# Optimization experiments

Measured on AMD Instinct MI355X. Metric: run time of the kernel, lower is better.

Reference implementation:

```python
import jax, jax.numpy as jnp
import numpy as np

N_GENES = 15135
K = int(np.ceil(0.5 * N_GENES))  # 7568, PyG TopKPooling ratio=0.5
BS, E, F_IN, H, HF, NC, L = 8, 242160, 64, 128, 512, 2, 3


def setup_inputs() -> dict:
    key = jax.random.key(0)
    ks = jax.random.split(key, 16)
    def lin(k, fin, fout):
        s = 1.0 / np.sqrt(fin)
        return jax.random.normal(k, (fin, fout), jnp.float32) * s
    x = jax.random.normal(ks[0], (BS, N_GENES, F_IN), jnp.float32)
    batch = jnp.zeros((BS,), jnp.int32)
    edge_index = jax.random.randint(ks[1], (2, E), 0, N_GENES, dtype=jnp.int32)
    CAT = L * H
    return {
        "x": x,
        "batch": batch,
        "edge_index": edge_index,
        "W1": lin(ks[2], F_IN, H), "b1": jnp.zeros((H,), jnp.float32),
        "W2": lin(ks[3], H, H),    "b2": jnp.zeros((H,), jnp.float32),
        "W3": lin(ks[4], H, H),    "b3": jnp.zeros((H,), jnp.float32),
        "topk_w": jax.random.normal(ks[5], (CAT,), jnp.float32) / np.sqrt(CAT),
        "fcW": lin(ks[6], CAT, 1), "fcb": jnp.zeros((1,), jnp.float32),
        "lin1W": lin(ks[7], K, HF), "lin1b": jnp.zeros((HF,), jnp.float32),
        "lin2W": lin(ks[8], HF, NC), "lin2b": jnp.zeros((NC,), jnp.float32),
    }


def reference(x, batch, edge_index, W1, b1, W2, b2, W3, b3,
              topk_w, fcW, fcb, lin1W, lin1b, lin2W, lin2b):
    bs = x.shape[0]
    # --- GCN normalization with self-loops (PyG GCNConv defaults) ---
    loop = jnp.arange(N_GENES, dtype=edge_index.dtype)
    src = jnp.concatenate([edge_index[0], loop])
    dst = jnp.concatenate([edge_index[1], loop])
    deg = jnp.zeros((N_GENES,), x.dtype).at[dst].add(1.0)
    dinv = jax.lax.rsqrt(deg)  # deg >= 1 due to self-loops
    norm = dinv[src] * dinv[dst]  # [E+N]

    def gcn(h, W, b):
        h = h @ W                                   # [bs, N, H]
        msg = h[:, src, :] * norm[None, :, None]    # gather + edge weight
        agg = jnp.zeros_like(h).at[:, dst, :].add(msg)  # scatter-add
        return agg + b

    h1 = jax.nn.relu(gcn(x, W1, b1))
    h2 = jax.nn.relu(gcn(h1, W2, b2))
    h3 = jax.nn.relu(gcn(h2, W3, b3))
    # mode='cat': stack on last dim then flatten -> feature order (H, layer)
    xc = jnp.stack([h1, h2, h3], -1).reshape(bs, N_GENES, -1)  # [bs, N, L*H]

    # --- TopKPooling (score = tanh(x.w/||w||), keep top ceil(0.5*N)) ---
    score = jnp.tanh((xc @ topk_w) / jnp.linalg.norm(topk_w))  # [bs, N]
    top_s, perm = jax.lax.top_k(score, K)                       # [bs, K]
    xp = jnp.take_along_axis(xc, perm[..., None], axis=1) * top_s[..., None]

    z = (xp @ fcW + fcb)[..., 0]          # [bs, K]
    h = jax.nn.relu(z @ lin1W + lin1b)    # [bs, HF]; dropout inactive (eval)
    logits = h @ lin2W + lin2b            # [bs, NC]
    return jax.nn.log_softmax(logits, axis=-1)
```

## Files before the change

### kernel.cpp

```cpp
#include <hip/hip_runtime.h>
#include <hip/hip_fp16.h>

#define N_G   15135
#define E_N   242160
#define BSZ   8
#define K_TOP 7568
#define NH    128
#define NBIN  65536
#define SUFS  65600

typedef float f4v __attribute__((ext_vector_type(4)));
typedef unsigned int u4v __attribute__((ext_vector_type(4)));

__global__ void zero_kernel(int* __restrict__ p, int n) {
  int i = blockIdx.x * 1024 + threadIdx.x;
  if (i < n) p[i] = 0;
}

__global__ void count_kernel(const int* __restrict__ ei, int* __restrict__ cnt) {
  int e = blockIdx.x * 256 + threadIdx.x;
  if (e < E_N) atomicAdd(&cnt[ei[E_N + e]], 1);
}

__global__ __launch_bounds__(1024) void scan_kernel(const int* __restrict__ cnt,
                                                    int* __restrict__ rowstart,
                                                    float* __restrict__ dinv,
                                                    int4* __restrict__ rowdesc,
                                                    int* __restrict__ gctr,
                                                    const float* __restrict__ topk_w,
                                                    float* __restrict__ scal) {
  __shared__ int buf[1024];
  __shared__ int base;
  int tid = threadIdx.x;
  int i = blockIdx.x * 1024 + tid;
  int v = (i < N_G) ? cnt[i] : 0;
  float di = 1.0f / sqrtf((float)(v + 1));
  if (i < N_G) dinv[i] = di;
  buf[tid] = v;
  __syncthreads();
  for (int s = 1; s < 1024; s <<= 1) {
    int t = (tid >= s) ? buf[tid - s] : 0;
    __syncthreads();
    buf[tid] += t;
    __syncthreads();
  }
  if (tid == 1023) base = atomicAdd(gctr, buf[1023]);
  __syncthreads();
  if (i < N_G) {
    int rs = base + buf[tid] - v;
    rowstart[i] = rs;
    rowdesc[i] = make_int4(rs, v, __float_as_int(di), 0);
  }
  if (blockIdx.x == 0) {
    __shared__ float fbuf[512];
    if (tid < 512) {
      float w = (tid < 384) ? topk_w[tid] : 0.f;
      fbuf[tid] = w * w;
    }
    __syncthreads();
    for (int s = 256; s > 0; s >>= 1) {
      if (tid < s) fbuf[tid] += fbuf[tid + s];
      __syncthreads();
    }
    if (tid == 0) scal[0] = 1.0f / sqrtf(fbuf[0]);
  }
}

__global__ void fill_kernel(const int* __restrict__ ei, const int* __restrict__ rowstart,
                            const float* __restrict__ dinv, int* __restrict__ fillc,
                            int2* __restrict__ csr) {
  int e = blockIdx.x * 256 + threadIdx.x;
  if (e < E_N) {
    int s = ei[e], d = ei[E_N + e];
    int pos = rowstart[d] + atomicAdd(&fillc[d], 1);
    csr[pos] = make_int2(s, __float_as_int(dinv[s]));
  }
}

template<int CIN, bool BR, bool H16>
__global__ __launch_bounds__(256, 6) void mm_kernel(const float* __restrict__ A,
                                                    const float* __restrict__ W,
                                                    const float* __restrict__ bias,
                                                    void* __restrict__ outv) {
  __shared__ float Bst[32][132];
  __shared__ float Ast2[32][68];
  int tid = threadIdx.x;
  int b = blockIdx.x & 7;
  int ib = blockIdx.x >> 3;
  int rb0 = b * N_G + ib * 64;
  int rmax = N_G - ib * 64;
  int c0 = (tid & 31) * 4;
  int r0 = (tid >> 5) * 8;
  float acc[8][4];
#pragma unroll
  for (int i = 0; i < 8; i++)
#pragma unroll
    for (int j = 0; j < 4; j++) acc[i][j] = 0.f;

  for (int k0 = 0; k0 < CIN; k0 += 32) {
    {
      int koff = (tid & 7) * 4;
      int row = tid >> 3;
#pragma unroll
      for (int p = 0; p < 2; ++p) {
        int r = row + p * 32;
        f4v v = {0.f, 0.f, 0.f, 0.f};
        if (r < rmax) v = __builtin_nontemporal_load((const f4v*)(A + (size_t)(rb0 + r) * CIN + k0 + koff));
        Ast2[koff + 0][r] = v.x; Ast2[koff + 1][r] = v.y;
        Ast2[koff + 2][r] = v.z; Ast2[koff + 3][r] = v.w;
      }
    }
    {
      int cc = (tid & 31) * 4;
      int kr = tid >> 5;
#pragma unroll
      for (int p = 0; p < 4; ++p) {
        int k = kr + p * 8;
        *(float4*)&Bst[k][cc] = *(const float4*)(W + (size_t)(k0 + k) * NH + cc);
      }
    }
    __syncthreads();
#pragma unroll 4
    for (int kk = 0; kk < 32; ++kk) {
      float a[8], bb[4];
      *(float4*)&a[0] = *(const float4*)&Ast2[kk][r0];
      *(float4*)&a[4] = *(const float4*)&Ast2[kk][r0 + 4];
      *(float4*)&bb[0] = *(const float4*)&Bst[kk][c0];
#pragma unroll
      for (int i = 0; i < 8; i++)
#pragma unroll
        for (int j = 0; j < 4; j++)
          acc[i][j] = fmaf(a[i], bb[j], acc[i][j]);
    }
    __syncthreads();
  }
  float b0 = 0.f, b1 = 0.f, b2 = 0.f, b3 = 0.f;
  if (BR) { b0 = bias[c0]; b1 = bias[c0+1]; b2 = bias[c0+2]; b3 = bias[c0+3]; }
#pragma unroll
  for (int i = 0; i < 8; i++) {
    int r = r0 + i;
    if (r < rmax) {
      if (H16) {
        __half2 pr[2];
        pr[0] = __floats2half2_rn(acc[i][0], acc[i][1]);
        pr[1] = __floats2half2_rn(acc[i][2], acc[i][3]);
        *(uint2*)((__half*)outv + (size_t)(rb0 + r) * NH + c0) = *(uint2*)pr;
      } else {
        float4 v;
        if (BR) {
          v.x = fmaxf(acc[i][0] + b0, 0.f); v.y = fmaxf(acc[i][1] + b1, 0.f);
          v.z = fmaxf(acc[i][2] + b2, 0.f); v.w = fmaxf(acc[i][3] + b3, 0.f);
        } else {
          v.x = acc[i][0]; v.y = acc[i][1]; v.z = acc[i][2]; v.w = acc[i][3];
        }
        *(float4*)((float*)outv + (size_t)(rb0 + r) * NH + c0) = v;
      }
    }
  }
}

__global__ __launch_bounds__(256) void agg64_f4_kernel(const float* __restrict__ src,
                                                       const int2* __restrict__ csr,
                                                       const int4* __restrict__ rowdesc,
                                                       float* __restrict__ dst) {
  int b = blockIdx.x & 7;
  int chunk = blockIdx.x >> 3;
  int wave = threadIdx.x >> 6, lane = threadIdx.x & 63;
  int d = chunk * 4 + wave;
  if (d >= N_G) return;
  d = __builtin_amdgcn_readfirstlane(d);
  int slot = lane >> 4, li = lane & 15;
  int4 rd = rowdesc[d];
  int n = rd.y;
  float dv = __int_as_float(rd.z);
  const float* sb = src + (size_t)b * N_G * 64;
  const int2* ce = csr + rd.x;
  auto sel4 = [&](int a0, int a1, int a2, int a3) {
    int s01 = (slot & 1) ? a1 : a0;
    int s23 = (slot & 1) ? a3 : a2;
    return (slot & 2) ? s23 : s01;
  };
  f4v acc0 = {0.f, 0.f, 0.f, 0.f}, acc1 = {0.f, 0.f, 0.f, 0.f};
  {
    f4v sv = *(const f4v*)(sb + (size_t)d * 64 + li * 4);
    float ws = (slot == 0) ? dv : 0.f;
    acc0.x = fmaf(ws, sv.x, acc0.x); acc0.y = fmaf(ws, sv.y, acc0.y);
    acc0.z = fmaf(ws, sv.z, acc0.z); acc0.w = fmaf(ws, sv.w, acc0.w);
  }
  int l = 0;
  for (; l + 8 <= n; l += 8) {
    int2 p[8];
#pragma unroll
    for (int k = 0; k < 8; ++k) p[k] = ce[l + k];
    int s0 = sel4(p[0].x, p[1].x, p[2].x, p[3].x);
    int s1 = sel4(p[4].x, p[5].x, p[6].x, p[7].x);
    float w0 = __int_as_float(sel4(p[0].y, p[1].y, p[2].y, p[3].y));
    float w1 = __int_as_float(sel4(p[4].y, p[5].y, p[6].y, p[7].y));
    f4v v0 = *(const f4v*)(sb + (size_t)s0 * 64 + li * 4);
    f4v v1 = *(const f4v*)(sb + (size_t)s1 * 64 + li * 4);
    acc0.x = fmaf(w0, v0.x, acc0.x); acc0.y = fmaf(w0, v0.y, acc0.y);
    acc0.z = fmaf(w0, v0.z, acc0.z); acc0.w = fmaf(w0, v0.w, acc0.w);
    acc1.x = fmaf(w1, v1.x, acc1.x); acc1.y = fmaf(w1, v1.y, acc1.y);
    acc1.z = fmaf(w1, v1.z, acc1.z); acc1.w = fmaf(w1, v1.w, acc1.w);
  }
  for (; l < n; ++l) {
    int2 p = ce[l];
    float w = (slot == 0) ? __int_as_float(p.y) : 0.f;
    f4v v = *(const f4v*)(sb + (size_t)p.x * 64 + li * 4);
    acc0.x = fmaf(w, v.x, acc0.x); acc0.y = fmaf(w, v.y, acc0.y);
    acc0.z = fmaf(w, v.z, acc0.z); acc0.w = fmaf(w, v.w, acc0.w);
  }
  f4v a;
  a.x = acc0.x + acc1.x; a.y = acc0.y + acc1.y;
  a.z = acc0.z + acc1.z; a.w = acc0.w + acc1.w;
  a.x += __shfl_xor(a.x, 16); a.y += __shfl_xor(a.y, 16);
  a.z += __shfl_xor(a.z, 16); a.w += __shfl_xor(a.w, 16);
  a.x += __shfl_xor(a.x, 32); a.y += __shfl_xor(a.y, 32);
  a.z += __shfl_xor(a.z, 32); a.w += __shfl_xor(a.w, 32);
  if (slot == 0) {
    f4v r;
    r.x = dv * a.x; r.y = dv * a.y; r.z = dv * a.z; r.w = dv * a.w;
    __builtin_nontemporal_store(r, (f4v*)(dst + ((size_t)b * N_G + d) * 64 + li * 4));
  }
}

__global__ __launch_bounds__(256) void agg128_f4_kernel(const float* __restrict__ hw,
                                                        const int2* __restrict__ csr,
                                                        const int4* __restrict__ rowdesc,
                                                        const float* __restrict__ bias,
                                                        float* __restrict__ hout) {
  int b = blockIdx.x & 7;
  int chunk = blockIdx.x >> 3;
  int wave = threadIdx.x >> 6, lane = threadIdx.x & 63;
  int d0 = chunk * 8 + wave * 2;
  if (d0 >= N_G) return;
  d0 = __builtin_amdgcn_readfirstlane(d0);
  int d1i = d0 + 1;
  int has1 = (d1i < N_G);
  int dB = has1 ? d1i : d0;
  int half = lane >> 5, li = lane & 31;
  int4 rdA = rowdesc[d0];
  int4 rdB = rowdesc[dB];
  int nA = rdA.y, nB = has1 ? rdB.y : 0;
  float dvA = __int_as_float(rdA.z);
  float dvB = __int_as_float(rdB.z);
  const float* sb = hw + (size_t)b * N_G * NH;
  const int2* ceA = csr + rdA.x;
  const int2* ceB = csr + rdB.x;
  auto sel2 = [&](int a0, int a1) { return half ? a1 : a0; };
  f4v aA0 = {0.f,0.f,0.f,0.f}, aA1 = {0.f,0.f,0.f,0.f};
  f4v aB0 = {0.f,0.f,0.f,0.f}, aB1 = {0.f,0.f,0.f,0.f};
  {
    f4v sv = *(const f4v*)(sb + (size_t)d0 * NH + li * 4);
    float ws = (half == 0) ? dvA : 0.f;
    aA0.x = fmaf(ws, sv.x, aA0.x); aA0.y = fmaf(ws, sv.y, aA0.y);
    aA0.z = fmaf(ws, sv.z, aA0.z); aA0.w = fmaf(ws, sv.w, aA0.w);
    f4v svb = *(const f4v*)(sb + (size_t)dB * NH + li * 4);
    float wsb = (half == 0 && has1) ? dvB : 0.f;
    aB0.x = fmaf(wsb, svb.x, aB0.x); aB0.y = fmaf(wsb, svb.y, aB0.y);
    aB0.z = fmaf(wsb, svb.z, aB0.z); aB0.w = fmaf(wsb, svb.w, aB0.w);
  }
  auto batch8 = [&](const int2* ce, int l, f4v& c0, f4v& c1) {
    int2 p[8];
#pragma unroll
    for (int k = 0; k < 8; ++k) p[k] = ce[l + k];
    int s0 = sel2(p[0].x, p[1].x), s1 = sel2(p[2].x, p[3].x);
    int s2 = sel2(p[4].x, p[5].x), s3 = sel2(p[6].x, p[7].x);
    float w0 = __int_as_float(sel2(p[0].y, p[1].y));
    float w1 = __int_as_float(sel2(p[2].y, p[3].y));
    float w2 = __int_as_float(sel2(p[4].y, p[5].y));
    float w3 = __int_as_float(sel2(p[6].y, p[7].y));
    f4v v0 = *(const f4v*)(sb + (size_t)s0 * NH + li * 4);
    f4v v1 = *(const f4v*)(sb + (size_t)s1 * NH + li * 4);
    f4v v2 = *(const f4v*)(sb + (size_t)s2 * NH + li * 4);
    f4v v3 = *(const f4v*)(sb + (size_t)s3 * NH + li * 4);
    c0.x = fmaf(w0, v0.x, c0.x); c0.y = fmaf(w0, v0.y, c0.y);
    c0.z = fmaf(w0, v0.z, c0.z); c0.w = fmaf(w0, v0.w, c0.w);
    c1.x = fmaf(w1, v1.x, c1.x); c1.y = fmaf(w1, v1.y, c1.y);
    c1.z = fmaf(w1, v1.z, c1.z); c1.w = fmaf(w1, v1.w, c1.w);
    c0.x = fmaf(w2, v2.x, c0.x); c0.y = fmaf(w2, v2.y, c0.y);
    c0.z = fmaf(w2, v2.z, c0.z); c0.w = fmaf(w2, v2.w, c0.w);
    c1.x = fmaf(w3, v3.x, c1.x); c1.y = fmaf(w3, v3.y, c1.y);
    c1.z = fmaf(w3, v3.z, c1.z); c1.w = fmaf(w3, v3.w, c1.w);
  };
  int lA = 0, lB = 0;
  while (lA + 8 <= nA && lB + 8 <= nB) {
    batch8(ceA, lA, aA0, aA1);
    batch8(ceB, lB, aB0, aB1);
    lA += 8; lB += 8;
  }
  for (; lA + 8 <= nA; lA += 8) batch8(ceA, lA, aA0, aA1);
  for (; lB + 8 <= nB; lB += 8) batch8(ceB, lB, aB0, aB1);
  while (lA < nA || lB < nB) {
    int hasA = (lA < nA), hasB = (lB < nB);
    int sA = hasA ? ceA[lA].x : d0;
    int wAi = hasA ? ceA[lA].y : 0;
    int sB = hasB ? ceB[lB].x : d0;
    int wBi = hasB ? ceB[lB].y : 0;
    int s = half ? sB : sA;
    float wa = (half == 0 && hasA) ? __int_as_float(wAi) : 0.f;
    float wb = (half == 1 && hasB) ? __int_as_float(wBi) : 0.f;
    f4v v = *(const f4v*)(sb + (size_t)s * NH + li * 4);
    aA0.x = fmaf(wa, v.x, aA0.x); aA0.y = fmaf(wa, v.y, aA0.y);
    aA0.z = fmaf(wa, v.z, aA0.z); aA0.w = fmaf(wa, v.w, aA0.w);
    aB0.x = fmaf(wb, v.x, aB0.x); aB0.y = fmaf(wb, v.y, aB0.y);
    aB0.z = fmaf(wb, v.z, aB0.z); aB0.w = fmaf(wb, v.w, aB0.w);
    lA += hasA; lB += hasB;
  }
  f4v aA, aB;
  aA.x = aA0.x + aA1.x; aA.y = aA0.y + aA1.y;
  aA.z = aA0.z + aA1.z; aA.w = aA0.w + aA1.w;
  aB.x = aB0.x + aB1.x; aB.y = aB0.y + aB1.y;
  aB.z = aB0.z + aB1.z; aB.w = aB0.w + aB1.w;
  aA.x += __shfl_xor(aA.x, 32); aA.y += __shfl_xor(aA.y, 32);
  aA.z += __shfl_xor(aA.z, 32); aA.w += __shfl_xor(aA.w, 32);
  aB.x += __shfl_xor(aB.x, 32); aB.y += __shfl_xor(aB.y, 32);
  aB.z += __shfl_xor(aB.z, 32); aB.w += __shfl_xor(aB.w, 32);

  f4v bb = *(const f4v*)(bias + li * 4);
  float dv = half ? dvB : dvA;
  f4v av;
  av.x = half ? aB.x : aA.x; av.y = half ? aB.y : aA.y;
  av.z = half ? aB.z : aA.z; av.w = half ? aB.w : aA.w;
  f4v r;
  r.x = fmaxf(fmaf(dv, av.x, bb.x), 0.f);
  r.y = fmaxf(fmaf(dv, av.y, bb.y), 0.f);
  r.z = fmaxf(fmaf(dv, av.z, bb.z), 0.f);
  r.w = fmaxf(fmaf(dv, av.w, bb.w), 0.f);
  int dsel = half ? dB : d0;
  if (half == 0 || has1)
    __builtin_nontemporal_store(r, (f4v*)(hout + ((size_t)b * N_G + dsel) * NH + li * 4));
}

__global__ __launch_bounds__(256) void agg128h_score_kernel(
    const __half* __restrict__ hwh,
    const int2* __restrict__ csr,
    const int4* __restrict__ rowdesc,
    const float* __restrict__ bias,
    const float* __restrict__ h1,
    const float* __restrict__ h2,
    const float* __restrict__ topk_w,
    const float* __restrict__ fcW,
    const float* __restrict__ scal,
    float* __restrict__ score,
    float* __restrict__ d2a,
    unsigned* __restrict__ keys,
    int* __restrict__ hist) {
  int b = blockIdx.x & 7;
  int chunk = blockIdx.x >> 3;
  int wave = threadIdx.x >> 6, lane = threadIdx.x & 63;
  int d = chunk * 4 + wave;
  if (d >= N_G) return;
  d = __builtin_amdgcn_readfirstlane(d);
  int slot = lane >> 4, li = lane & 15;
  int4 rd = rowdesc[d];
  int n = rd.y;
  float dv = __int_as_float(rd.z);
  const __half* sb = hwh + (size_t)b * N_G * NH;
  const int2* ce = csr + rd.x;
  auto sel4 = [&](int a0, int a1, int a2, int a3) {
    int s01 = (slot & 1) ? a1 : a0;
    int s23 = (slot & 1) ? a3 : a2;
    return (slot & 2) ? s23 : s01;
  };
  float a0[8], a1[8];
#pragma unroll
  for (int j = 0; j < 8; ++j) { a0[j] = 0.f; a1[j] = 0.f; }
  auto gacc = [&](int s, float w, float* acc) {
    u4v raw = *(const u4v*)(sb + (size_t)s * NH + li * 8);
    unsigned q0 = raw.x, q1 = raw.y, q2 = raw.z, q3 = raw.w;
    float2 f0 = __half22float2(*(const __half2*)&q0);
    float2 f1 = __half22float2(*(const __half2*)&q1);
    float2 f2 = __half22float2(*(const __half2*)&q2);
    float2 f3 = __half22float2(*(const __half2*)&q3);
    acc[0] = fmaf(w, f0.x, acc[0]); acc[1] = fmaf(w, f0.y, acc[1]);
    acc[2] = fmaf(w, f1.x, acc[2]); acc[3] = fmaf(w, f1.y, acc[3]);
    acc[4] = fmaf(w, f2.x, acc[4]); acc[5] = fmaf(w, f2.y, acc[5]);
    acc[6] = fmaf(w, f3.x, acc[6]); acc[7] = fmaf(w, f3.y, acc[7]);
  };
  gacc(d, (slot == 0) ? dv : 0.f, a0);
  int l = 0;
  for (; l + 8 <= n; l += 8) {
    int2 p[8];
#pragma unroll
    for (int k = 0; k < 8; ++k) p[k] = ce[l + k];
    int s0 = sel4(p[0].x, p[1].x, p[2].x, p[3].x);
    int s1 = sel4(p[4].x, p[5].x, p[6].x, p[7].x);
    float w0 = __int_as_float(sel4(p[0].y, p[1].y, p[2].y, p[3].y));
    float w1 = __int_as_float(sel4(p[4].y, p[5].y, p[6].y, p[7].y));
    gacc(s0, w0, a0);
    gacc(s1, w1, a1);
  }
  for (; l < n; ++l) {
    int2 p = ce[l];
    gacc(p.x, (slot == 0) ? __int_as_float(p.y) : 0.f, a0);
  }
  float a[8];
#pragma unroll
  for (int j = 0; j < 8; ++j) {
    a[j] = a0[j] + a1[j];
    a[j] += __shfl_xor(a[j], 16);
    a[j] += __shfl_xor(a[j], 32);
  }
  size_t rb = ((size_t)b * N_G + d) * NH + li * 8;
  f4v u1a = __builtin_nontemporal_load((const f4v*)(h1 + rb));
  f4v u1b = __builtin_nontemporal_load((const f4v*)(h1 + rb + 4));
  f4v u2a = __builtin_nontemporal_load((const f4v*)(h2 + rb));
  f4v u2b = __builtin_nontemporal_load((const f4v*)(h2 + rb + 4));
  f4v bba = *(const f4v*)(bias + li * 8);
  f4v bbb = *(const f4v*)(bias + li * 8 + 4);
  float r[8];
  r[0] = fmaxf(fmaf(dv, a[0], bba.x), 0.f);
  r[1] = fmaxf(fmaf(dv, a[1], bba.y), 0.f);
  r[2] = fmaxf(fmaf(dv, a[2], bba.z), 0.f);
  r[3] = fmaxf(fmaf(dv, a[3], bba.w), 0.f);
  r[4] = fmaxf(fmaf(dv, a[4], bbb.x), 0.f);
  r[5] = fmaxf(fmaf(dv, a[5], bbb.y), 0.f);
  r[6] = fmaxf(fmaf(dv, a[6], bbb.z), 0.f);
  r[7] = fmaxf(fmaf(dv, a[7], bbb.w), 0.f);
  float u1[8] = {u1a.x, u1a.y, u1a.z, u1a.w, u1b.x, u1b.y, u1b.z, u1b.w};
  float u2[8] = {u2a.x, u2a.y, u2a.z, u2a.w, u2b.x, u2b.y, u2b.z, u2b.w};
  const float* tw = topk_w + li * 24;
  const float* fw = fcW + li * 24;
  float d1 = 0.f, d2 = 0.f;
#pragma unroll
  for (int j = 0; j < 8; ++j) {
    d1 += u1[j] * tw[j * 3] + u2[j] * tw[j * 3 + 1] + r[j] * tw[j * 3 + 2];
    d2 += u1[j] * fw[j * 3] + u2[j] * fw[j * 3 + 1] + r[j] * fw[j * 3 + 2];
  }
#pragma unroll
  for (int sh = 8; sh > 0; sh >>= 1) {
    d1 += __shfl_down(d1, sh, 16);
    d2 += __shfl_down(d2, sh, 16);
  }
  if (lane == 0) {
    int gw = b * N_G + d;
    float scv = tanhf(d1 * scal[0]);
    score[gw] = scv;
    d2a[gw] = d2;
    unsigned u = __float_as_uint(scv);
    unsigned k32 = (u & 0x80000000u) ? ~u : (u | 0x80000000u);
    keys[gw] = k32;
    atomicAdd(&hist[b * NBIN + (int)(k32 >> 16)], 1);
  }
}

__global__ __launch_bounds__(1024) void suffix_kernel(const int* __restrict__ hist,
                                                      int* __restrict__ suf) {
  __shared__ int buf[1024];
  int b = blockIdx.x;
  const int* hb = hist + b * NBIN;
  int* sb = suf + b * SUFS;
  int t = threadIdx.x;
  int base = t * 64;
  int s = 0;
  for (int k = 0; k < 64; ++k) s += hb[base + k];
  buf[t] = s;
  __syncthreads();
  for (int off = 1; off < 1024; off <<= 1) {
    int v = (t + off < 1024) ? buf[t + off] : 0;
    __syncthreads();
    buf[t] += v;
    __syncthreads();
  }
  int acc = buf[t] - s;
  if (t == 0) sb[NBIN] = 0;
  for (int k = 63; k >= 0; --k) {
    acc += hb[base + k];
    sb[base + k] = acc;
  }
}

__global__ void scatter_kernel(const unsigned* __restrict__ keys, int* __restrict__ hist,
                               const int* __restrict__ suf, int2* __restrict__ bucket) {
  int b = blockIdx.y;
  int i = blockIdx.x * 256 + threadIdx.x;
  if (i >= N_G) return;
  unsigned k = keys[b * N_G + i];
  int bin = (int)(k >> 16);
  int old = atomicSub(&hist[b * NBIN + bin], 1);
  int pos = suf[b * SUFS + bin + 1] + old - 1;
  bucket[b * N_G + pos] = make_int2((int)k, i);
}

__global__ void rank_z_kernel(const unsigned* __restrict__ keys, const int* __restrict__ suf,
                              const int2* __restrict__ bucket, const float* __restrict__ score,
                              const float* __restrict__ d2a, const float* __restrict__ fcb,
                              float* __restrict__ z) {
  int b = blockIdx.y;
  int i = blockIdx.x * 256 + threadIdx.x;
  if (i >= N_G) return;
  int gw = b * N_G + i;
  unsigned k = keys[gw];
  int bin = (int)(k >> 16);
  int lo = suf[b * SUFS + bin + 1];
  int hi = suf[b * SUFS + bin];
  int r = lo;
  const int2* bk = bucket + b * N_G;
  for (int p = lo; p < hi; ++p) {
    int2 e = bk[p];
    unsigned kj = (unsigned)e.x;
    r += (kj > k || (kj == k && e.y < i)) ? 1 : 0;
  }
  if (r < K_TOP) z[b * K_TOP + r] = fmaf(score[gw], d2a[gw], fcb[0]);
}

__global__ __launch_bounds__(256) void lin1_kernel(const float* __restrict__ z,
                                                   const float* __restrict__ W,
                                                   float* __restrict__ hpre) {
  __shared__ float zb[8][237];
  int rs = blockIdx.x;
  int r0 = rs * 237;
  int rn = K_TOP - r0; if (rn > 237) rn = 237;
  for (int t = threadIdx.x; t < 8 * rn; t += 256) {
    int bb = t / rn, rr = t - bb * rn;
    zb[bb][rr] = z[bb * K_TOP + r0 + rr];
  }
  __syncthreads();
  int c = threadIdx.x;
  float a[8][2];
#pragma unroll
  for (int bb = 0; bb < 8; ++bb) { a[bb][0] = 0.f; a[bb][1] = 0.f; }
  for (int r = 0; r < rn; ++r) {
    const float* wr = W + (size_t)(r0 + r) * 512;
    float w0 = wr[c], w1 = wr[c + 256];
#pragma unroll
    for (int bb = 0; bb < 8; ++bb) {
      float zz = zb[bb][r];
      a[bb][0] = fmaf(zz, w0, a[bb][0]);
      a[bb][1] = fmaf(zz, w1, a[bb][1]);
    }
  }
#pragma unroll
  for (int bb = 0; bb < 8; ++bb) {
    atomicAdd(&hpre[bb * 512 + c], a[bb][0]);
    atomicAdd(&hpre[bb * 512 + c + 256], a[bb][1]);
  }
}

__global__ __launch_bounds__(128) void lin2_kernel(const float* __restrict__ hpre,
                                                   const float* __restrict__ l1b,
                                                   const float* __restrict__ W2,
                                                   const float* __restrict__ l2b,
                                                   float* __restrict__ out) {
  int b = blockIdx.x, tid = threadIdx.x;
  float a0 = 0.f, a1 = 0.f;
  for (int j = tid; j < 512; j += 128) {
    float t = fmaxf(hpre[b * 512 + j] + l1b[j], 0.f);
    a0 = fmaf(t, W2[j * 2 + 0], a0);
    a1 = fmaf(t, W2[j * 2 + 1], a1);
  }
#pragma unroll
  for (int s = 32; s > 0; s >>= 1) {
    a0 += __shfl_down(a0, s);
    a1 += __shfl_down(a1, s);
  }
  __shared__ float red[2][2];
  if ((tid & 63) == 0) { red[tid >> 6][0] = a0; red[tid >> 6][1] = a1; }
  __syncthreads();
  if (tid == 0) {
    float l0 = red[0][0] + red[1][0] + l2b[0];
    float l1 = red[0][1] + red[1][1] + l2b[1];
    float m = fmaxf(l0, l1);
    float lse = m + logf(expf(l0 - m) + expf(l1 - m));
    out[b * 2 + 0] = l0 - lse;
    out[b * 2 + 1] = l1 - lse;
  }
}

extern "C" void kernel_launch(void* const* d_in, const int* in_sizes, int n_in,
                              void* d_out, int out_size, void* d_ws, size_t ws_size,
                              hipStream_t stream) {
  const float* x   = (const float*)d_in[0];
  const int*   ei  = (const int*)d_in[2];
  const float* W1  = (const float*)d_in[3];
  const float* b1  = (const float*)d_in[4];
  const float* W2  = (const float*)d_in[5];
  const float* b2  = (const float*)d_in[6];
  const float* W3  = (const float*)d_in[7];
  const float* b3  = (const float*)d_in[8];
  const float* tkw = (const float*)d_in[9];
  const float* fcW = (const float*)d_in[10];
  const float* fcb = (const float*)d_in[11];
  const float* l1W = (const float*)d_in[12];
  const float* l1b = (const float*)d_in[13];
  const float* l2W = (const float*)d_in[14];
  const float* l2b = (const float*)d_in[15];
  float* out = (float*)d_out;

  char* ws = (char*)d_ws;
  size_t off = 0;
  auto alloc = [&](size_t bytes) {
    char* p = ws + off;
    off += (bytes + 255) & ~(size_t)255;
    return p;
  };
  int*   cnt   = (int*)alloc(15136 * 4);
  int*   fillc = (int*)alloc(15136 * 4);
  int*   gctr  = (int*)alloc(256);
  float* hpre  = (float*)alloc(4096 * 4);
  int*   hist  = (int*)alloc((size_t)BSZ * NBIN * 4);
  int*   rowstart = (int*)alloc(15136 * 4);
  float* dinv  = (float*)alloc(15136 * 4);
  int4*  rowdesc = (int4*)alloc(15136 * 16);
  float* scal  = (float*)alloc(64);
  float* z     = (float*)alloc((size_t)BSZ * K_TOP * 4);
  float* score = (float*)alloc(121088 * 4);
  float* d2a   = (float*)alloc(121088 * 4);
  unsigned* keys = (unsigned*)alloc(121088 * 4);
  int*   suf   = (int*)alloc((size_t)BSZ * SUFS * 4);
  int2*  bucket = (int2*)alloc(121088 * 8);
  int2*  csr   = (int2*)alloc((size_t)E_N * 8);
  float* ax = (float*)alloc((size_t)BSZ * N_G * 64 * 4);
  float* hw = (float*)alloc((size_t)BSZ * N_G * NH * 4);
  float* h1 = (float*)alloc((size_t)BSZ * N_G * NH * 4);
  float* h2 = (float*)alloc((size_t)BSZ * N_G * NH * 4);
  (void)ws_size; (void)in_sizes; (void)n_in; (void)out_size;

  int zero_n = (int)(((char*)rowstart - (char*)cnt) / 4);
  zero_kernel<<<(zero_n + 1023) / 1024, 1024, 0, stream>>>(cnt, zero_n);
  count_kernel<<<(E_N + 255) / 256, 256, 0, stream>>>(ei, cnt);
  scan_kernel<<<(N_G + 1023) / 1024, 1024, 0, stream>>>(cnt, rowstart, dinv, rowdesc, gctr, tkw, scal);
  fill_kernel<<<(E_N + 255) / 256, 256, 0, stream>>>(ei, rowstart, dinv, fillc, csr);

  dim3 mmg(8 * 237);
  int aggblocks  = 8 * ((N_G + 3) / 4);
  int aggblocks2 = 8 * ((N_G + 7) / 8);

  agg64_f4_kernel<<<aggblocks, 256, 0, stream>>>(x, csr, rowdesc, ax);
  mm_kernel<64, true, false><<<mmg, 256, 0, stream>>>(ax, W1, b1, h1);
  mm_kernel<128, false, false><<<mmg, 256, 0, stream>>>(h1, W2, nullptr, hw);
  agg128_f4_kernel<<<aggblocks2, 256, 0, stream>>>(hw, csr, rowdesc, b2, h2);
  mm_kernel<128, false, true><<<mmg, 256, 0, stream>>>(h2, W3, nullptr, hw);
  agg128h_score_kernel<<<aggblocks, 256, 0, stream>>>((const __half*)hw, csr, rowdesc, b3,
                                                      h1, h2, tkw, fcW, scal,
                                                      score, d2a, keys, hist);

  dim3 ng((N_G + 255) / 256, BSZ);
  suffix_kernel<<<BSZ, 1024, 0, stream>>>(hist, suf);
  scatter_kernel<<<ng, 256, 0, stream>>>(keys, hist, suf, bucket);
  rank_z_kernel<<<ng, 256, 0, stream>>>(keys, suf, bucket, score, d2a, fcb, z);

  lin1_kernel<<<32, 256, 0, stream>>>(z, l1W, hpre);
  lin2_kernel<<<BSZ, 128, 0, stream>>>(hpre, l1b, l2W, l2b, out);
}
```

Measured before the change: 650.8 us.

## Restructure edge-gather mapping in layer-1 and layer-3 aggregation kernels

The layer-1 aggregation now gives each lane one scalar feature per edge instead of splitting edges across 16-lane slots. It also software-pipelines the gathers, loading the next 8 neighbor rows before accumulating the current 8, which removes the cross-slot shuffle reductions. The layer-3 half-precision aggregation plus score kernel now processes two destination nodes per wave, one per 32-lane half, using 8-byte half loads and half the grid, mirroring the layer-2 kernel. The aim is more memory-level parallelism and fewer shuffles per node, at the cost of more registers and divergent tail handling when the two nodes have different degrees.

```diff
diff --git a/kernel.cpp b/kernel.cpp
--- a/kernel.cpp
+++ b/kernel.cpp
@@ -10,7 +10,7 @@
 #define SUFS  65600
 
 typedef float f4v __attribute__((ext_vector_type(4)));
-typedef unsigned int u4v __attribute__((ext_vector_type(4)));
+typedef unsigned int u2v __attribute__((ext_vector_type(2)));
 
 __global__ void zero_kernel(int* __restrict__ p, int n) {
   int i = blockIdx.x * 1024 + threadIdx.x;
@@ -159,69 +159,53 @@
   }
 }
 
-__global__ __launch_bounds__(256) void agg64_f4_kernel(const float* __restrict__ src,
-                                                       const int2* __restrict__ csr,
-                                                       const int4* __restrict__ rowdesc,
-                                                       float* __restrict__ dst) {
+__global__ __launch_bounds__(256) void agg64_kernel(const float* __restrict__ src,
+                                                    const int2* __restrict__ csr,
+                                                    const int4* __restrict__ rowdesc,
+                                                    float* __restrict__ dst) {
   int b = blockIdx.x & 7;
   int chunk = blockIdx.x >> 3;
   int wave = threadIdx.x >> 6, lane = threadIdx.x & 63;
   int d = chunk * 4 + wave;
   if (d >= N_G) return;
   d = __builtin_amdgcn_readfirstlane(d);
-  int slot = lane >> 4, li = lane & 15;
   int4 rd = rowdesc[d];
-  int n = rd.y;
+  int e0 = rd.x, n = rd.y;
   float dv = __int_as_float(rd.z);
   const float* sb = src + (size_t)b * N_G * 64;
-  const int2* ce = csr + rd.x;
-  auto sel4 = [&](int a0, int a1, int a2, int a3) {
-    int s01 = (slot & 1) ? a1 : a0;
-    int s23 = (slot & 1) ? a3 : a2;
-    return (slot & 2) ? s23 : s01;
-  };
-  f4v acc0 = {0.f, 0.f, 0.f, 0.f}, acc1 = {0.f, 0.f, 0.f, 0.f};
-  {
-    f4v sv = *(const f4v*)(sb + (size_t)d * 64 + li * 4);
-    float ws = (slot == 0) ? dv : 0.f;
-    acc0.x = fmaf(ws, sv.x, acc0.x); acc0.y = fmaf(ws, sv.y, acc0.y);
-    acc0.z = fmaf(ws, sv.z, acc0.z); acc0.w = fmaf(ws, sv.w, acc0.w);
-  }
+  const int2* ce = csr + e0;
+  float acc[8];
+  acc[0] = dv * sb[(size_t)d * 64 + lane];
+#pragma unroll
+  for (int k = 1; k < 8; ++k) acc[k] = 0.f;
   int l = 0;
-  for (; l + 8 <= n; l += 8) {
-    int2 p[8];
-#pragma unroll
-    for (int k = 0; k < 8; ++k) p[k] = ce[l + k];
-    int s0 = sel4(p[0].x, p[1].x, p[2].x, p[3].x);
-    int s1 = sel4(p[4].x, p[5].x, p[6].x, p[7].x);
-    float w0 = __int_as_float(sel4(p[0].y, p[1].y, p[2].y, p[3].y));
-    float w1 = __int_as_float(sel4(p[4].y, p[5].y, p[6].y, p[7].y));
-    f4v v0 = *(const f4v*)(sb + (size_t)s0 * 64 + li * 4);
-    f4v v1 = *(const f4v*)(sb + (size_t)s1 * 64 + li * 4);
-    acc0.x = fmaf(w0, v0.x, acc0.x); acc0.y = fmaf(w0, v0.y, acc0.y);
-    acc0.z = fmaf(w0, v0.z, acc0.z); acc0.w = fmaf(w0, v0.w, acc0.w);
-    acc1.x = fmaf(w1, v1.x, acc1.x); acc1.y = fmaf(w1, v1.y, acc1.y);
-    acc1.z = fmaf(w1, v1.z, acc1.z); acc1.w = fmaf(w1, v1.w, acc1.w);
+  if (n >= 8) {
+    int2 pA[8]; float vA[8];
+#pragma unroll
+    for (int k = 0; k < 8; ++k) pA[k] = ce[k];
+#pragma unroll
+    for (int k = 0; k < 8; ++k) vA[k] = sb[(size_t)pA[k].x * 64 + lane];
+    l = 8;
+    for (; l + 8 <= n; l += 8) {
+      int2 pB[8]; float vB[8];
+#pragma unroll
+      for (int k = 0; k < 8; ++k) pB[k] = ce[l + k];
+#pragma unroll
+      for (int k = 0; k < 8; ++k) vB[k] = sb[(size_t)pB[k].x * 64 + lane];
+#pragma unroll
+      for (int k = 0; k < 8; ++k) acc[k] = fmaf(__int_as_float(pA[k].y), vA[k], acc[k]);
+#pragma unroll
+      for (int k = 0; k < 8; ++k) { pA[k] = pB[k]; vA[k] = vB[k]; }
+    }
+#pragma unroll
+    for (int k = 0; k < 8; ++k) acc[k] = fmaf(__int_as_float(pA[k].y), vA[k], acc[k]);
   }
   for (; l < n; ++l) {
     int2 p = ce[l];
-    float w = (slot == 0) ? __int_as_float(p.y) : 0.f;
-    f4v v = *(const f4v*)(sb + (size_t)p.x * 64 + li * 4);
-    acc0.x = fmaf(w, v.x, acc0.x); acc0.y = fmaf(w, v.y, acc0.y);
-    acc0.z = fmaf(w, v.z, acc0.z); acc0.w = fmaf(w, v.w, acc0.w);
-  }
-  f4v a;
-  a.x = acc0.x + acc1.x; a.y = acc0.y + acc1.y;
-  a.z = acc0.z + acc1.z; a.w = acc0.w + acc1.w;
-  a.x += __shfl_xor(a.x, 16); a.y += __shfl_xor(a.y, 16);
-  a.z += __shfl_xor(a.z, 16); a.w += __shfl_xor(a.w, 16);
-  a.x += __shfl_xor(a.x, 32); a.y += __shfl_xor(a.y, 32);
-  a.z += __shfl_xor(a.z, 32); a.w += __shfl_xor(a.w, 32);
-  if (slot == 0) {
-    f4v r;
-    r.x = dv * a.x; r.y = dv * a.y; r.z = dv * a.z; r.w = dv * a.w;
-    __builtin_nontemporal_store(r, (f4v*)(dst + ((size_t)b * N_G + d) * 64 + li * 4));
-  }
+    acc[0] = fmaf(__int_as_float(p.y), sb[(size_t)p.x * 64 + lane], acc[0]);
+  }
+  float s = ((acc[0] + acc[1]) + (acc[2] + acc[3])) + ((acc[4] + acc[5]) + (acc[6] + acc[7]));
+  __builtin_nontemporal_store(dv * s, &dst[((size_t)b * N_G + d) * 64 + lane]);
 }
 
 __global__ __launch_bounds__(256) void agg128_f4_kernel(const float* __restrict__ hw,
@@ -332,7 +316,7 @@
     __builtin_nontemporal_store(r, (f4v*)(hout + ((size_t)b * N_G + dsel) * NH + li * 4));
 }
 
-__global__ __launch_bounds__(256) void agg128h_score_kernel(
+__global__ __launch_bounds__(256) void agg128h2_score_kernel(
     const __half* __restrict__ hwh,
     const int2* __restrict__ csr,
     const int4* __restrict__ rowdesc,
@@ -349,92 +333,133 @@
   int b = blockIdx.x & 7;
   int chunk = blockIdx.x >> 3;
   int wave = threadIdx.x >> 6, lane = threadIdx.x & 63;
-  int d = chunk * 4 + wave;
-  if (d >= N_G) return;
-  d = __builtin_amdgcn_readfirstlane(d);
-  int slot = lane >> 4, li = lane & 15;
-  int4 rd = rowdesc[d];
-  int n = rd.y;
-  float dv = __int_as_float(rd.z);
+  int d0 = chunk * 8 + wave * 2;
+  if (d0 >= N_G) return;
+  d0 = __builtin_amdgcn_readfirstlane(d0);
+  int d1i = d0 + 1;
+  int has1 = (d1i < N_G);
+  int dB = has1 ? d1i : d0;
+  int half = lane >> 5, li = lane & 31;
+  int4 rdA = rowdesc[d0];
+  int4 rdB = rowdesc[dB];
+  int nA = rdA.y, nB = has1 ? rdB.y : 0;
+  float dvA = __int_as_float(rdA.z);
+  float dvB = __int_as_float(rdB.z);
   const __half* sb = hwh + (size_t)b * N_G * NH;
-  const int2* ce = csr + rd.x;
-  auto sel4 = [&](int a0, int a1, int a2, int a3) {
-    int s01 = (slot & 1) ? a1 : a0;
-    int s23 = (slot & 1) ? a3 : a2;
-    return (slot & 2) ? s23 : s01;
-  };
-  float a0[8], a1[8];
-#pragma unroll
-  for (int j = 0; j < 8; ++j) { a0[j] = 0.f; a1[j] = 0.f; }
-  auto gacc = [&](int s, float w, float* acc) {
-    u4v raw = *(const u4v*)(sb + (size_t)s * NH + li * 8);
-    unsigned q0 = raw.x, q1 = raw.y, q2 = raw.z, q3 = raw.w;
+  const int2* ceA = csr + rdA.x;
+  const int2* ceB = csr + rdB.x;
+  auto sel2 = [&](int a0, int a1) { return half ? a1 : a0; };
+  auto h2f = [](u2v raw) {
+    unsigned q0 = raw.x, q1 = raw.y;
     float2 f0 = __half22float2(*(const __half2*)&q0);
     float2 f1 = __half22float2(*(const __half2*)&q1);
-    float2 f2 = __half22float2(*(const __half2*)&q2);
-    float2 f3 = __half22float2(*(const __half2*)&q3);
-    acc[0] = fmaf(w, f0.x, acc[0]); acc[1] = fmaf(w, f0.y, acc[1]);
-    acc[2] = fmaf(w, f1.x, acc[2]); acc[3] = fmaf(w, f1.y, acc[3]);
-    acc[4] = fmaf(w, f2.x, acc[4]); acc[5] = fmaf(w, f2.y, acc[5]);
-    acc[6] = fmaf(w, f3.x, acc[6]); acc[7] = fmaf(w, f3.y, acc[7]);
+    f4v v; v.x = f0.x; v.y = f0.y; v.z = f1.x; v.w = f1.y;
+    return v;
   };
-  gacc(d, (slot == 0) ? dv : 0.f, a0);
-  int l = 0;
-  for (; l + 8 <= n; l += 8) {
+  f4v aA0 = {0.f,0.f,0.f,0.f}, aA1 = {0.f,0.f,0.f,0.f};
+  f4v aB0 = {0.f,0.f,0.f,0.f}, aB1 = {0.f,0.f,0.f,0.f};
+  {
+    f4v sv = h2f(*(const u2v*)(sb + (size_t)d0 * NH + li * 4));
+    float ws = (half == 0) ? dvA : 0.f;
+    aA0.x = fmaf(ws, sv.x, aA0.x); aA0.y = fmaf(ws, sv.y, aA0.y);
+    aA0.z = fmaf(ws, sv.z, aA0.z); aA0.w = fmaf(ws, sv.w, aA0.w);
+    f4v svb = h2f(*(const u2v*)(sb + (size_t)dB * NH + li * 4));
+    float wsb = (half == 0 && has1) ? dvB : 0.f;
+    aB0.x = fmaf(wsb, svb.x, aB0.x); aB0.y = fmaf(wsb, svb.y, aB0.y);
+    aB0.z = fmaf(wsb, svb.z, aB0.z); aB0.w = fmaf(wsb, svb.w, aB0.w);
+  }
+  auto batch8 = [&](const int2* ce, int l, f4v& c0, f4v& c1) {
     int2 p[8];
 #pragma unroll
     for (int k = 0; k < 8; ++k) p[k] = ce[l + k];
-    int s0 = sel4(p[0].x, p[1].x, p[2].x, p[3].x);
-    int s1 = sel4(p[4].x, p[5].x, p[6].x, p[7].x);
-    float w0 = __int_as_float(sel4(p[0].y, p[1].y, p[2].y, p[3].y));
-    float w1 = __int_as_float(sel4(p[4].y, p[5].y, p[6].y, p[7].y));
-    gacc(s0, w0, a0);
-    gacc(s1, w1, a1);
-  }
-  for (; l < n; ++l) {
-    int2 p = ce[l];
-    gacc(p.x, (slot == 0) ? __int_as_float(p.y) : 0.f, a0);
-  }
-  float a[8];
-#pragma unroll
-  for (int j = 0; j < 8; ++j) {
-    a[j] = a0[j] + a1[j];
-    a[j] += __shfl_xor(a[j], 16);
-    a[j] += __shfl_xor(a[j], 32);
-  }
-  size_t rb = ((size_t)b * N_G + d) * NH + li * 8;
-  f4v u1a = __builtin_nontemporal_load((const f4v*)(h1 + rb));
-  f4v u1b = __builtin_nontemporal_load((const f4v*)(h1 + rb + 4));
-  f4v u2a = __builtin_nontemporal_load((const f4v*)(h2 + rb));
-  f4v u2b = __builtin_nontemporal_load((const f4v*)(h2 + rb + 4));
-  f4v bba = *(const f4v*)(bias + li * 8);
-  f4v bbb = *(const f4v*)(bias + li * 8 + 4);
-  float r[8];
-  r[0] = fmaxf(fmaf(dv, a[0], bba.x), 0.f);
-  r[1] = fmaxf(fmaf(dv, a[1], bba.y), 0.f);
-  r[2] = fmaxf(fmaf(dv, a[2], bba.z), 0.f);
-  r[3] = fmaxf(fmaf(dv, a[3], bba.w), 0.f);
-  r[4] = fmaxf(fmaf(dv, a[4], bbb.x), 0.f);
-  r[5] = fmaxf(fmaf(dv, a[5], bbb.y), 0.f);
-  r[6] = fmaxf(fmaf(dv, a[6], bbb.z), 0.f);
-  r[7] = fmaxf(fmaf(dv, a[7], bbb.w), 0.f);
-  float u1[8] = {u1a.x, u1a.y, u1a.z, u1a.w, u1b.x, u1b.y, u1b.z, u1b.w};
-  float u2[8] = {u2a.x, u2a.y, u2a.z, u2a.w, u2b.x, u2b.y, u2b.z, u2b.w};
-  const float* tw = topk_w + li * 24;
-  const float* fw = fcW + li * 24;
-  float d1 = 0.f, d2 = 0.f;
-#pragma unroll
-  for (int j = 0; j < 8; ++j) {
-    d1 += u1[j] * tw[j * 3] + u2[j] * tw[j * 3 + 1] + r[j] * tw[j * 3 + 2];
-    d2 += u1[j] * fw[j * 3] + u2[j] * fw[j * 3 + 1] + r[j] * fw[j * 3 + 2];
-  }
-#pragma unroll
-  for (int sh = 8; sh > 0; sh >>= 1) {
-    d1 += __shfl_down(d1, sh, 16);
-    d2 += __shfl_down(d2, sh, 16);
-  }
-  if (lane == 0) {
-    int gw = b * N_G + d;
+    int s0 = sel2(p[0].x, p[1].x), s1 = sel2(p[2].x, p[3].x);
+    int s2 = sel2(p[4].x, p[5].x), s3 = sel2(p[6].x, p[7].x);
+    float w0 = __int_as_float(sel2(p[0].y, p[1].y));
+    float w1 = __int_as_float(sel2(p[2].y, p[3].y));
+    float w2 = __int_as_float(sel2(p[4].y, p[5].y));
+    float w3 = __int_as_float(sel2(p[6].y, p[7].y));
+    u2v r0 = *(const u2v*)(sb + (size_t)s0 * NH + li * 4);
+    u2v r1 = *(const u2v*)(sb + (size_t)s1 * NH + li * 4);
+    u2v r2 = *(const u2v*)(sb + (size_t)s2 * NH + li * 4);
+    u2v r3 = *(const u2v*)(sb + (size_t)s3 * NH + li * 4);
+    f4v v0 = h2f(r0), v1 = h2f(r1), v2 = h2f(r2), v3 = h2f(r3);
+    c0.x = fmaf(w0, v0.x, c0.x); c0.y = fmaf(w0, v0.y, c0.y);
+    c0.z = fmaf(w0, v0.z, c0.z); c0.w = fmaf(w0, v0.w, c0.w);
+    c1.x = fmaf(w1, v1.x, c1.x); c1.y = fmaf(w1, v1.y, c1.y);
+    c1.z = fmaf(w1, v1.z, c1.z); c1.w = fmaf(w1, v1.w, c1.w);
+    c0.x = fmaf(w2, v2.x, c0.x); c0.y = fmaf(w2, v2.y, c0.y);
+    c0.z = fmaf(w2, v2.z, c0.z); c0.w = fmaf(w2, v2.w, c0.w);
+    c1.x = fmaf(w3, v3.x, c1.x); c1.y = fmaf(w3, v3.y, c1.y);
+    c1.z = fmaf(w3, v3.z, c1.z); c1.w = fmaf(w3, v3.w, c1.w);
+  };
+  int lA = 0, lB = 0;
+  while (lA + 8 <= nA && lB + 8 <= nB) {
+    batch8(ceA, lA, aA0, aA1);
+    batch8(ceB, lB, aB0, aB1);
+    lA += 8; lB += 8;
+  }
+  for (; lA + 8 <= nA; lA += 8) batch8(ceA, lA, aA0, aA1);
+  for (; lB + 8 <= nB; lB += 8) batch8(ceB, lB, aB0, aB1);
+  while (lA < nA || lB < nB) {
+    int hasA = (lA < nA), hasB = (lB < nB);
+    int sA = hasA ? ceA[lA].x : d0;
+    int wAi = hasA ? ceA[lA].y : 0;
+    int sB = hasB ? ceB[lB].x : d0;
+    int wBi = hasB ? ceB[lB].y : 0;
+    int s = half ? sB : sA;
+    float wa = (half == 0 && hasA) ? __int_as_float(wAi) : 0.f;
+    float wb = (half == 1 && hasB) ? __int_as_float(wBi) : 0.f;
+    f4v v = h2f(*(const u2v*)(sb + (size_t)s * NH + li * 4));
+    aA0.x = fmaf(wa, v.x, aA0.x); aA0.y = fmaf(wa, v.y, aA0.y);
+    aA0.z = fmaf(wa, v.z, aA0.z); aA0.w = fmaf(wa, v.w, aA0.w);
+    aB0.x = fmaf(wb, v.x, aB0.x); aB0.y = fmaf(wb, v.y, aB0.y);
+    aB0.z = fmaf(wb, v.z, aB0.z); aB0.w = fmaf(wb, v.w, aB0.w);
+    lA += hasA; lB += hasB;
+  }
+  f4v aA, aB;
+  aA.x = aA0.x + aA1.x; aA.y = aA0.y + aA1.y;
+  aA.z = aA0.z + aA1.z; aA.w = aA0.w + aA1.w;
+  aB.x = aB0.x + aB1.x; aB.y = aB0.y + aB1.y;
+  aB.z = aB0.z + aB1.z; aB.w = aB0.w + aB1.w;
+  aA.x += __shfl_xor(aA.x, 32); aA.y += __shfl_xor(aA.y, 32);
+  aA.z += __shfl_xor(aA.z, 32); aA.w += __shfl_xor(aA.w, 32);
+  aB.x += __shfl_xor(aB.x, 32); aB.y += __shfl_xor(aB.y, 32);
+  aB.z += __shfl_xor(aB.z, 32); aB.w += __shfl_xor(aB.w, 32);
+
+  f4v bb = *(const f4v*)(bias + li * 4);
+  float dv = half ? dvB : dvA;
+  f4v av;
+  av.x = half ? aB.x : aA.x; av.y = half ? aB.y : aA.y;
+  av.z = half ? aB.z : aA.z; av.w = half ? aB.w : aA.w;
+  f4v r;
+  r.x = fmaxf(fmaf(dv, av.x, bb.x), 0.f);
+  r.y = fmaxf(fmaf(dv, av.y, bb.y), 0.f);
+  r.z = fmaxf(fmaf(dv, av.z, bb.z), 0.f);
+  r.w = fmaxf(fmaf(dv, av.w, bb.w), 0.f);
+  int dsel = half ? dB : d0;
+
+  size_t rb = ((size_t)b * N_G + dsel) * NH + li * 4;
+  f4v u1 = __builtin_nontemporal_load((const f4v*)(h1 + rb));
+  f4v u2 = __builtin_nontemporal_load((const f4v*)(h2 + rb));
+  const float* twp = topk_w + li * 12;
+  const float* fwp = fcW + li * 12;
+  f4v ta = *(const f4v*)(twp + 0), tb2 = *(const f4v*)(twp + 4), tc = *(const f4v*)(twp + 8);
+  f4v fa = *(const f4v*)(fwp + 0), fb = *(const f4v*)(fwp + 4), fc = *(const f4v*)(fwp + 8);
+  float d1 = u1.x * ta.x + u2.x * ta.y + r.x * ta.z
+           + u1.y * ta.w + u2.y * tb2.x + r.y * tb2.y
+           + u1.z * tb2.z + u2.z * tb2.w + r.z * tc.x
+           + u1.w * tc.y + u2.w * tc.z + r.w * tc.w;
+  float d2 = u1.x * fa.x + u2.x * fa.y + r.x * fa.z
+           + u1.y * fa.w + u2.y * fb.x + r.y * fb.y
+           + u1.z * fb.z + u2.z * fb.w + r.z * fc.x
+           + u1.w * fc.y + u2.w * fc.z + r.w * fc.w;
+#pragma unroll
+  for (int sh = 16; sh > 0; sh >>= 1) {
+    d1 += __shfl_down(d1, sh, 32);
+    d2 += __shfl_down(d2, sh, 32);
+  }
+  if (li == 0 && (half == 0 || has1)) {
+    int gw = b * N_G + dsel;
     float scv = tanhf(d1 * scal[0]);
     score[gw] = scv;
     d2a[gw] = d2;
@@ -627,14 +652,14 @@
   int aggblocks  = 8 * ((N_G + 3) / 4);
   int aggblocks2 = 8 * ((N_G + 7) / 8);
 
-  agg64_f4_kernel<<<aggblocks, 256, 0, stream>>>(x, csr, rowdesc, ax);
+  agg64_kernel<<<aggblocks, 256, 0, stream>>>(x, csr, rowdesc, ax);
   mm_kernel<64, true, false><<<mmg, 256, 0, stream>>>(ax, W1, b1, h1);
   mm_kernel<128, false, false><<<mmg, 256, 0, stream>>>(h1, W2, nullptr, hw);
   agg128_f4_kernel<<<aggblocks2, 256, 0, stream>>>(hw, csr, rowdesc, b2, h2);
   mm_kernel<128, false, true><<<mmg, 256, 0, stream>>>(h2, W3, nullptr, hw);
-  agg128h_score_kernel<<<aggblocks, 256, 0, stream>>>((const __half*)hw, csr, rowdesc, b3,
-                                                      h1, h2, tkw, fcW, scal,
-                                                      score, d2a, keys, hist);
+  agg128h2_score_kernel<<<aggblocks2, 256, 0, stream>>>((const __half*)hw, csr, rowdesc, b3,
+                                                        h1, h2, tkw, fcW, scal,
+                                                        score, d2a, keys, hist);
 
   dim3 ng((N_G + 255) / 256, BSZ);
   suffix_kernel<<<BSZ, 1024, 0, stream>>>(hist, suf);
```

Result: faster. 598.0 us (-8.1%).
